# Kernel optimization log

Hardware: AMD Instinct MI355X
Metric: run time of the kernel (lower is better)

The kernel has to match this reference:

```python
import jax, jax.numpy as jnp
import numpy as np

EMBED = 256
HEADS = 8
LEVELS = 4
POINTS = 4
HEAD_DIM = EMBED // HEADS
SHAPES = [(100, 100), (50, 50), (25, 25), (13, 13)]  # (H, W) per level
NUM_KEYS = sum(h * w for h, w in SHAPES)  # 13294
LEVEL_STARTS = np.cumsum([0] + [h * w for h, w in SHAPES])[:-1]
B, Q = 8, 900


def _offset_bias():
    # Faithful reproduction of the torch _reset_parameters sampling_offsets bias.
    th = np.arange(HEADS, dtype=np.float32) * (2.0 * np.pi / HEADS)
    g = np.stack([np.cos(th), np.sin(th)], -1)
    g = g / np.abs(g).max(-1, keepdims=True)
    g = np.tile(g[:, None, None, :], (1, LEVELS, POINTS, 1))
    g = g * np.arange(1, POINTS + 1, dtype=np.float32)[None, None, :, None]
    return jnp.asarray(g.reshape(-1), dtype=jnp.float32)


def setup_inputs() -> dict:
    key = jax.random.key(0)
    ks = jax.random.split(key, 12)
    s = 1.0 / np.sqrt(EMBED)
    return {
        "query": jax.random.normal(ks[0], (B, Q, EMBED), jnp.float32),
        "reference_points": jax.random.uniform(ks[1], (B, Q, LEVELS, 2), jnp.float32),
        "value": jax.random.normal(ks[2], (B, NUM_KEYS, EMBED), jnp.float32),
        "spatial_shapes": jnp.asarray(np.array(SHAPES, dtype=np.int32)),
        "level_start_index": jnp.asarray(LEVEL_STARTS.astype(np.int32)),
        "W_off": jax.random.normal(ks[3], (EMBED, HEADS * LEVELS * POINTS * 2), jnp.float32) * 0.01,
        "b_off": _offset_bias(),
        "W_attn": jax.random.normal(ks[4], (EMBED, HEADS * LEVELS * POINTS), jnp.float32) * 0.01,
        "b_attn": jnp.zeros((HEADS * LEVELS * POINTS,), jnp.float32),
        "W_val": jax.random.normal(ks[5], (EMBED, EMBED), jnp.float32) * s,
        "b_val": jnp.zeros((EMBED,), jnp.float32),
        "W_out": jax.random.normal(ks[6], (EMBED, EMBED), jnp.float32) * s,
        "b_out": jnp.zeros((EMBED,), jnp.float32),
    }


def _bilinear(vflat, x, y, H, W):
    # vflat: [BH, H*W, D]; x, y: [BH, Q, P] in unnormalized pixel coords.
    # grid_sample(mode='bilinear', padding_mode='zeros', align_corners=False)
    BH, Qn, Pn = x.shape
    D = vflat.shape[-1]
    x0f = jnp.floor(x); y0f = jnp.floor(y)
    wx = x - x0f; wy = y - y0f
    x0 = x0f.astype(jnp.int32); y0 = y0f.astype(jnp.int32)

    def gather(xi, yi):
        inb = (xi >= 0) & (xi < W) & (yi >= 0) & (yi < H)
        idx = jnp.clip(yi, 0, H - 1) * W + jnp.clip(xi, 0, W - 1)
        g = jnp.take_along_axis(vflat, idx.reshape(BH, Qn * Pn, 1), axis=1)
        return g.reshape(BH, Qn, Pn, D) * inb[..., None].astype(vflat.dtype)

    v00 = gather(x0, y0)
    v01 = gather(x0 + 1, y0)
    v10 = gather(x0, y0 + 1)
    v11 = gather(x0 + 1, y0 + 1)
    return (v00 * ((1 - wx) * (1 - wy))[..., None]
            + v01 * (wx * (1 - wy))[..., None]
            + v10 * ((1 - wx) * wy)[..., None]
            + v11 * (wx * wy)[..., None])


def _msda(value_hd, shapes_np, starts_np, loc, attw):
    # value_hd: [B, K, H, D]; loc: [B, Q, H, L, P, 2]; attw: [B, Q, H, L, P]
    Bn, K, Hn, D = value_hd.shape
    Qn, Pn = loc.shape[1], loc.shape[4]
    out = jnp.zeros((Bn * Hn, Qn, D), value_hd.dtype)
    for l, (Hl, Wl) in enumerate(shapes_np):
        s = int(starts_np[l])
        v = value_hd[:, s:s + Hl * Wl]                      # [B, Hl*Wl, H, D]
        v = v.reshape(Bn, Hl * Wl, Hn, D).transpose(0, 2, 1, 3)
        vflat = v.reshape(Bn * Hn, Hl * Wl, D)
        # sampling_grid = 2*loc - 1; grid_sample align_corners=False -> x = loc*W - 0.5
        lx = loc[:, :, :, l, :, 0].transpose(0, 2, 1, 3).reshape(Bn * Hn, Qn, Pn)
        ly = loc[:, :, :, l, :, 1].transpose(0, 2, 1, 3).reshape(Bn * Hn, Qn, Pn)
        samp = _bilinear(vflat, lx * Wl - 0.5, ly * Hl - 0.5, Hl, Wl)  # [BH,Q,P,D]
        w = attw[:, :, :, l, :].transpose(0, 2, 1, 3).reshape(Bn * Hn, Qn, Pn)
        out = out + jnp.einsum('bqpd,bqp->bqd', samp, w)
    return out.reshape(Bn, Hn, Qn, D).transpose(0, 2, 1, 3).reshape(Bn, Qn, Hn * D)


def reference(query, reference_points, value, spatial_shapes, level_start_index,
              W_off, b_off, W_attn, b_attn, W_val, b_val, W_out, b_out):
    shapes_np = np.asarray(spatial_shapes)
    starts_np = np.asarray(level_start_index)
    Bn, Qn, _ = query.shape
    K = value.shape[1]

    v = value @ W_val + b_val                              # [B, K, E]
    v = v.reshape(Bn, K, HEADS, HEAD_DIM)

    off = (query @ W_off + b_off).reshape(Bn, Qn, HEADS, LEVELS, POINTS, 2)
    aw = (query @ W_attn + b_attn).reshape(Bn, Qn, HEADS, LEVELS * POINTS)
    aw = jax.nn.softmax(aw, axis=-1).reshape(Bn, Qn, HEADS, LEVELS, POINTS)

    # offset_normalizer = (W, H) per level
    norm = jnp.asarray(shapes_np[:, ::-1].astype(np.float32)).reshape(1, 1, 1, LEVELS, 1, 2)
    loc = reference_points[:, :, None, :, None, :] + off / norm  # [B,Q,H,L,P,2]

    out = _msda(v, shapes_np, starts_np, loc, aw)          # [B, Q, E]
    return out @ W_out + b_out
```

## Files before the change

### kernel.cpp

```cpp
#include <hip/hip_runtime.h>
#include <hip/hip_bf16.h>
#include <math.h>
#include <type_traits>

#define BATCH 8
#define QLEN 900
#define HEADS 8
#define LEVELS 4
#define POINTS 4
#define NUM_KEYS 13294
#define BQ (BATCH * QLEN)
#define MROWS_V (BATCH * NUM_KEYS)

__constant__ const int c_LH[4] = {100, 50, 25, 13};
__constant__ const int c_LW[4] = {100, 50, 25, 13};
__constant__ const int c_LS[4] = {0, 10000, 12500, 13125};

typedef __attribute__((ext_vector_type(8))) short bfrag;
typedef __attribute__((ext_vector_type(4))) float ffrag;

static __device__ __forceinline__ unsigned short f2bf(float f) {
    __hip_bfloat16 h = __float2bfloat16(f);
    return *(unsigned short*)&h;
}
static __device__ __forceinline__ float bf2f(unsigned int u16) {
    unsigned int v = u16 << 16;
    float f;
    __builtin_memcpy(&f, &v, 4);
    return f;
}

__global__ __launch_bounds__(256)
void prep_kernel(const float* __restrict__ W_val, const float* __restrict__ W_off,
                 const float* __restrict__ W_attn, const float* __restrict__ W_out,
                 const float* __restrict__ b_off, const float* __restrict__ b_attn,
                 unsigned short* __restrict__ Wv, unsigned short* __restrict__ Woa,
                 unsigned short* __restrict__ Wo, float* __restrict__ boa) {
    const int id = blockIdx.x * 256 + threadIdx.x;
    if (id < 65536) {
        const int n = id >> 8, k = id & 255;
        Wv[id] = f2bf(W_val[k * 256 + n]);
    } else if (id < 131072) {
        const int t = id - 65536;
        const int n = t >> 8, k = t & 255;
        Woa[t] = f2bf(W_off[k * 256 + n]);
    } else if (id < 163840) {
        const int t = id - 131072;
        const int n = t >> 8, k = t & 255;
        Woa[65536 + t] = f2bf(W_attn[k * 128 + n]);
    } else if (id < 229376) {
        const int t = id - 163840;
        const int n = t >> 8, k = t & 255;
        Wo[t] = f2bf(W_out[k * 256 + n]);
    } else if (id < 229760) {
        const int t = id - 229376;
        boa[t] = (t < 256) ? b_off[t] : b_attn[t - 256];
    }
}

#define GST 72

template <typename AT, typename CT>
__global__ __launch_bounds__(256)
void gemm_mfma(const AT* __restrict__ A, const unsigned short* __restrict__ WT,
               const float* __restrict__ bias, CT* __restrict__ C,
               int M, int ldc) {
    __shared__ unsigned short As[64 * GST];
    __shared__ unsigned short Bs[128 * GST];
    const int tid = threadIdx.x;
    const int wave = tid >> 6;
    const int lane = tid & 63;
    const int ln = lane & 15;
    const int quad = lane >> 4;
    const int m0 = blockIdx.x * 64;
    const int n0 = blockIdx.y * 128;

    ffrag acc[8];
#pragma unroll
    for (int j = 0; j < 8; ++j) acc[j] = (ffrag){0.f, 0.f, 0.f, 0.f};

    const int ar = tid >> 2;
    const int akc = (tid & 3) * 16;
    const int brow = tid >> 1;
    const int bkc = (tid & 1) * 32;
    const bool a_ok = (m0 + ar) < M;
    const AT* a_src = A + (size_t)(m0 + ar) * 256 + akc;
    const unsigned short* b_src = WT + (size_t)(n0 + brow) * 256 + bkc;

    for (int k0 = 0; k0 < 256; k0 += 64) {
        unsigned short* adst = &As[ar * GST + akc];
        if constexpr (std::is_same<AT, float>::value) {
            float4 f0, f1, f2, f3;
            if (a_ok) {
                const float4* p = (const float4*)(a_src + k0);
                f0 = p[0]; f1 = p[1]; f2 = p[2]; f3 = p[3];
            } else {
                f0 = make_float4(0.f, 0.f, 0.f, 0.f);
                f1 = f0; f2 = f0; f3 = f0;
            }
            float v[16] = {f0.x, f0.y, f0.z, f0.w, f1.x, f1.y, f1.z, f1.w,
                           f2.x, f2.y, f2.z, f2.w, f3.x, f3.y, f3.z, f3.w};
            unsigned short u[16];
#pragma unroll
            for (int i = 0; i < 16; ++i) u[i] = f2bf(v[i]);
            ((uint4*)adst)[0] = ((uint4*)u)[0];
            ((uint4*)adst)[1] = ((uint4*)u)[1];
        } else {
            uint4 u0, u1;
            if (a_ok) {
                const uint4* p = (const uint4*)(a_src + k0);
                u0 = p[0]; u1 = p[1];
            } else {
                u0 = make_uint4(0, 0, 0, 0);
                u1 = u0;
            }
            ((uint4*)adst)[0] = u0;
            ((uint4*)adst)[1] = u1;
        }
        {
            const uint4* src = (const uint4*)(b_src + k0);
            uint4* dst = (uint4*)&Bs[brow * GST + bkc];
#pragma unroll
            for (int i = 0; i < 4; ++i) dst[i] = src[i];
        }
        __syncthreads();

#pragma unroll
        for (int ks = 0; ks < 2; ++ks) {
            const int koff = ks * 32 + quad * 8;
            bfrag af = *(const bfrag*)&As[(wave * 16 + ln) * GST + koff];
#pragma unroll
            for (int j = 0; j < 8; ++j) {
                bfrag bf = *(const bfrag*)&Bs[(j * 16 + ln) * GST + koff];
                acc[j] = __builtin_amdgcn_mfma_f32_16x16x32_bf16(af, bf, acc[j], 0, 0, 0);
            }
        }
        __syncthreads();
    }

#pragma unroll
    for (int j = 0; j < 8; ++j) {
        const int col = n0 + j * 16 + ln;
        const float bb = bias[col];
#pragma unroll
        for (int r = 0; r < 4; ++r) {
            const int row = m0 + wave * 16 + quad * 4 + r;
            if (row < M) {
                const float v = acc[j][r] + bb;
                if constexpr (std::is_same<CT, unsigned short>::value) {
                    C[(size_t)row * ldc + col] = f2bf(v);
                } else {
                    C[(size_t)row * ldc + col] = v;
                }
            }
        }
    }
}

__global__ __launch_bounds__(256, 4)
void msda_sample_kernel(const float* __restrict__ offattn,
                        const float* __restrict__ rp,
                        const unsigned short* __restrict__ vb,
                        unsigned short* __restrict__ outb) {
    const int bq0 = blockIdx.x * 8;
    const int tid = threadIdx.x;

    __shared__ float s_w[8][128];
    __shared__ float s_x[8][128];
    __shared__ float s_y[8][128];

#pragma unroll
    for (int i = 0; i < 4; ++i) {
        const int e = i * 256 + tid;
        const int q = e >> 7, t = e & 127;
        s_w[q][t] = offattn[(size_t)(bq0 + q) * 384 + 256 + t];
    }
    __syncthreads();

    if (tid < 64) {
        const int q = tid >> 3, h = tid & 7;
        float m = -1e30f;
#pragma unroll
        for (int i = 0; i < 16; ++i) m = fmaxf(m, s_w[q][h * 16 + i]);
        float e[16];
        float s = 0.f;
#pragma unroll
        for (int i = 0; i < 16; ++i) {
            e[i] = expf(s_w[q][h * 16 + i] - m);
            s += e[i];
        }
        const float inv = 1.f / s;
#pragma unroll
        for (int i = 0; i < 16; ++i) s_w[q][h * 16 + i] = e[i] * inv;
    }

#pragma unroll
    for (int i = 0; i < 4; ++i) {
        const int e = i * 256 + tid;
        const int q = e >> 7, t = e & 127;
        const int h = t >> 4, l = (t >> 2) & 3, p = t & 3;
        const int bq = bq0 + q;
        const float2 off = *(const float2*)(offattn + (size_t)bq * 384 + h * 32 + l * 8 + p * 2);
        const float Wl = (float)c_LW[l];
        const float Hl = (float)c_LH[l];
        const float rx = rp[((size_t)bq * 4 + l) * 2 + 0];
        const float ry = rp[((size_t)bq * 4 + l) * 2 + 1];
        s_x[q][t] = (rx + off.x / Wl) * Wl - 0.5f;
        s_y[q][t] = (ry + off.y / Hl) * Hl - 0.5f;
    }
    __syncthreads();

    const int q = tid >> 5;
    const int s = tid & 31;
    const int h = s >> 2;
    const int dp = s & 3;
    const int bq = bq0 + q;
    const int b = bq / QLEN;
    const unsigned short* vbase = vb + (size_t)b * NUM_KEYS * 256 + h * 32 + dp * 8;

    float acc[8];
#pragma unroll
    for (int d = 0; d < 8; ++d) acc[d] = 0.f;

#pragma unroll
    for (int l = 0; l < LEVELS; ++l) {
        const int Hl = c_LH[l];
        const int Wl = c_LW[l];
        const int s0 = c_LS[l];
#pragma unroll 2
        for (int p = 0; p < POINTS; ++p) {
            const int t2 = h * 16 + l * 4 + p;
            const float x = s_x[q][t2];
            const float y = s_y[q][t2];
            const float w = s_w[q][t2];
            const float x0f = floorf(x);
            const float y0f = floorf(y);
            const float wx = x - x0f;
            const float wy = y - y0f;
            const int x0 = (int)x0f;
            const int y0 = (int)y0f;
            const float mx0 = ((unsigned)x0 < (unsigned)Wl) ? 1.f : 0.f;
            const float mx1 = ((unsigned)(x0 + 1) < (unsigned)Wl) ? 1.f : 0.f;
            const float my0 = ((unsigned)y0 < (unsigned)Hl) ? 1.f : 0.f;
            const float my1 = ((unsigned)(y0 + 1) < (unsigned)Hl) ? 1.f : 0.f;
            const int xc0 = min(max(x0, 0), Wl - 1);
            const int xc1 = min(max(x0 + 1, 0), Wl - 1);
            const int yc0 = min(max(y0, 0), Hl - 1);
            const int yc1 = min(max(y0 + 1, 0), Hl - 1);
            const float a00 = w * (1.f - wx) * (1.f - wy) * mx0 * my0;
            const float a01 = w * wx * (1.f - wy) * mx1 * my0;
            const float a10 = w * (1.f - wx) * wy * mx0 * my1;
            const float a11 = w * wx * wy * mx1 * my1;
            const size_t k00 = (size_t)(s0 + yc0 * Wl + xc0) * 256;
            const size_t k01 = (size_t)(s0 + yc0 * Wl + xc1) * 256;
            const size_t k10 = (size_t)(s0 + yc1 * Wl + xc0) * 256;
            const size_t k11 = (size_t)(s0 + yc1 * Wl + xc1) * 256;
            const uint4 r00 = *(const uint4*)(vbase + k00);
            const uint4 r01 = *(const uint4*)(vbase + k01);
            const uint4 r10 = *(const uint4*)(vbase + k10);
            const uint4 r11 = *(const uint4*)(vbase + k11);
            const unsigned int w00[4] = {r00.x, r00.y, r00.z, r00.w};
            const unsigned int w01[4] = {r01.x, r01.y, r01.z, r01.w};
            const unsigned int w10[4] = {r10.x, r10.y, r10.z, r10.w};
            const unsigned int w11[4] = {r11.x, r11.y, r11.z, r11.w};
#pragma unroll
            for (int i = 0; i < 4; ++i) {
                const float v00l = bf2f(w00[i] & 0xffffu), v00h = bf2f(w00[i] >> 16);
                const float v01l = bf2f(w01[i] & 0xffffu), v01h = bf2f(w01[i] >> 16);
                const float v10l = bf2f(w10[i] & 0xffffu), v10h = bf2f(w10[i] >> 16);
                const float v11l = bf2f(w11[i] & 0xffffu), v11h = bf2f(w11[i] >> 16);
                acc[i * 2 + 0] = fmaf(a00, v00l, fmaf(a01, v01l, fmaf(a10, v10l, fmaf(a11, v11l, acc[i * 2 + 0]))));
                acc[i * 2 + 1] = fmaf(a00, v00h, fmaf(a01, v01h, fmaf(a10, v10h, fmaf(a11, v11h, acc[i * 2 + 1]))));
            }
        }
    }

    unsigned short o[8];
#pragma unroll
    for (int d = 0; d < 8; ++d) o[d] = f2bf(acc[d]);
    *(uint4*)(outb + (size_t)bq * 256 + h * 32 + dp * 8) = *(uint4*)o;
}

extern "C" void kernel_launch(void* const* d_in, const int* in_sizes, int n_in,
                              void* d_out, int out_size, void* d_ws, size_t ws_size,
                              hipStream_t stream) {
    const float* query  = (const float*)d_in[0];
    const float* rp     = (const float*)d_in[1];
    const float* value  = (const float*)d_in[2];
    const float* W_off  = (const float*)d_in[5];
    const float* b_off  = (const float*)d_in[6];
    const float* W_attn = (const float*)d_in[7];
    const float* b_attn = (const float*)d_in[8];
    const float* W_val  = (const float*)d_in[9];
    const float* b_val  = (const float*)d_in[10];
    const float* W_out  = (const float*)d_in[11];
    const float* b_out  = (const float*)d_in[12];
    float* out = (float*)d_out;

    char* w = (char*)d_ws;
    unsigned short* ws_vb = (unsigned short*)w;
    w += (size_t)MROWS_V * 256 * 2;
    float* ws_offattn = (float*)w;
    w += (size_t)BQ * 384 * 4;
    unsigned short* ws_msda = (unsigned short*)w;
    w += (size_t)BQ * 256 * 2;
    unsigned short* ws_Wv = (unsigned short*)w;  w += 256 * 256 * 2;
    unsigned short* ws_Woa = (unsigned short*)w; w += 384 * 256 * 2;
    unsigned short* ws_Wo = (unsigned short*)w;  w += 256 * 256 * 2;
    float* ws_boa = (float*)w;

    prep_kernel<<<898, 256, 0, stream>>>(W_val, W_off, W_attn, W_out,
                                         b_off, b_attn, ws_Wv, ws_Woa, ws_Wo, ws_boa);

    {
        dim3 grid((MROWS_V + 63) / 64, 2);
        gemm_mfma<float, unsigned short><<<grid, 256, 0, stream>>>(
            value, ws_Wv, b_val, ws_vb, MROWS_V, 256);
    }
    {
        dim3 grid((BQ + 63) / 64, 3);
        gemm_mfma<float, float><<<grid, 256, 0, stream>>>(
            query, ws_Woa, ws_boa, ws_offattn, BQ, 384);
    }
    msda_sample_kernel<<<BQ / 8, 256, 0, stream>>>(ws_offattn, rp, ws_vb, ws_msda);

    {
        dim3 grid((BQ + 63) / 64, 2);
        gemm_mfma<unsigned short, float><<<grid, 256, 0, stream>>>(
            ws_msda, ws_Wo, b_out, out, BQ, 256);
    }
}
```

Measured before the change: 280.6 us.

## Replace value projection GEMM with persistent register-resident weight streaming kernel

Adds a persistent kernel for the value projection in which each wave keeps its 64-column slice of the bf16 weight matrix in registers. Blocks loop over 16-row tiles in a grid-stride fashion, prefetching the next tile's fp32 activations while the current tile runs its MFMAs. This removes LDS staging and the repeated weight loads of the tiled GEMM, and it covers the whole N=256 width in one pass instead of two grid columns. In exchange it uses many registers, and each thread writes its bf16 outputs as scattered 2-byte stores.

```diff
diff --git a/kernel.cpp b/kernel.cpp
--- a/kernel.cpp
+++ b/kernel.cpp
@@ -55,6 +55,87 @@
     } else if (id < 229760) {
         const int t = id - 229376;
         boa[t] = (t < 256) ? b_off[t] : b_attn[t - 256];
+    }
+}
+
+#define VS_GRID 512
+
+__global__ __launch_bounds__(256, 2)
+void gemm_val_stream(const float* __restrict__ A, const unsigned short* __restrict__ WT,
+                     const float* __restrict__ bias, unsigned short* __restrict__ C,
+                     int M) {
+    const int tid = threadIdx.x;
+    const int wave = tid >> 6;
+    const int lane = tid & 63;
+    const int ln = lane & 15;
+    const int quad = lane >> 4;
+    const int n0 = wave * 64;
+
+    bfrag b[4][8];
+#pragma unroll
+    for (int j = 0; j < 4; ++j) {
+        const unsigned short* bp = WT + (size_t)(n0 + j * 16 + ln) * 256 + quad * 8;
+#pragma unroll
+        for (int ks = 0; ks < 8; ++ks)
+            b[j][ks] = *(const bfrag*)(bp + ks * 32);
+    }
+
+    const int ntiles = M >> 4;
+    int tile = blockIdx.x;
+    if (tile >= ntiles) return;
+
+    float4 f[8][2];
+    {
+        const float* ap = A + (size_t)(tile * 16 + ln) * 256 + quad * 8;
+#pragma unroll
+        for (int ks = 0; ks < 8; ++ks) {
+            f[ks][0] = *(const float4*)(ap + ks * 32);
+            f[ks][1] = *(const float4*)(ap + ks * 32 + 4);
+        }
+    }
+
+    while (tile < ntiles) {
+        bfrag a[8];
+#pragma unroll
+        for (int ks = 0; ks < 8; ++ks) {
+            const float v[8] = {f[ks][0].x, f[ks][0].y, f[ks][0].z, f[ks][0].w,
+                                f[ks][1].x, f[ks][1].y, f[ks][1].z, f[ks][1].w};
+#pragma unroll
+            for (int i = 0; i < 8; ++i) a[ks][i] = (short)f2bf(v[i]);
+        }
+
+        const int next = tile + VS_GRID;
+        const int pn = (next < ntiles) ? next : tile;
+        {
+            const float* ap = A + (size_t)(pn * 16 + ln) * 256 + quad * 8;
+#pragma unroll
+            for (int ks = 0; ks < 8; ++ks) {
+                f[ks][0] = *(const float4*)(ap + ks * 32);
+                f[ks][1] = *(const float4*)(ap + ks * 32 + 4);
+            }
+        }
+
+        ffrag acc[4];
+#pragma unroll
+        for (int j = 0; j < 4; ++j) acc[j] = (ffrag){0.f, 0.f, 0.f, 0.f};
+#pragma unroll
+        for (int ks = 0; ks < 8; ++ks) {
+#pragma unroll
+            for (int j = 0; j < 4; ++j)
+                acc[j] = __builtin_amdgcn_mfma_f32_16x16x32_bf16(a[ks], b[j][ks], acc[j], 0, 0, 0);
+        }
+
+        const int rb = tile * 16;
+#pragma unroll
+        for (int j = 0; j < 4; ++j) {
+            const int col = n0 + j * 16 + ln;
+            const float bb = bias[col];
+#pragma unroll
+            for (int r = 0; r < 4; ++r) {
+                C[(size_t)(rb + quad * 4 + r) * 256 + col] = f2bf(acc[j][r] + bb);
+            }
+        }
+        tile = next;
     }
 }
 
@@ -312,11 +393,8 @@
     prep_kernel<<<898, 256, 0, stream>>>(W_val, W_off, W_attn, W_out,
                                          b_off, b_attn, ws_Wv, ws_Woa, ws_Wo, ws_boa);
 
-    {
-        dim3 grid((MROWS_V + 63) / 64, 2);
-        gemm_mfma<float, unsigned short><<<grid, 256, 0, stream>>>(
-            value, ws_Wv, b_val, ws_vb, MROWS_V, 256);
-    }
+    gemm_val_stream<<<VS_GRID, 256, 0, stream>>>(value, ws_Wv, b_val, ws_vb, MROWS_V);
+
     {
         dim3 grid((BQ + 63) / 64, 3);
         gemm_mfma<float, float><<<grid, 256, 0, stream>>>(
```

Result: faster. 274.7 us (-2.1%).
